# Performance work log

Hardware: AMD Instinct MI355X
Metric: run time of the kernel (lower is better)

Reference implementation:

```python
import jax, jax.numpy as jnp
import numpy as np

NUM_NODES = 100000
NUM_EDGES = 1600000
HID = 128
NODE_DIM = 5
MSG_DIM = 2


def _mlp(x, params):
    # 3 hidden ReLU layers + linear head, matching nn.Sequential in torch
    (W0, b0, W1, b1, W2, b2, W3, b3) = params
    h = jax.nn.relu(x @ W0 + b0)
    h = jax.nn.relu(h @ W1 + b1)
    h = jax.nn.relu(h @ W2 + b2)
    return h @ W3 + b3


def setup_inputs() -> dict:
    key = jax.random.key(0)
    ks = jax.random.split(key, 12)
    nodes = jax.random.normal(ks[0], (NUM_NODES, NODE_DIM), dtype=jnp.float32)
    edge_index = jax.random.randint(ks[1], (2, NUM_EDGES), 0, NUM_NODES, dtype=jnp.int32)

    def lin(k, fan_in, fan_out):
        # kaiming-uniform-ish init, scale irrelevant for correctness baseline
        bound = 1.0 / np.sqrt(fan_in)
        return jax.random.uniform(k, (fan_in, fan_out), jnp.float32, -bound, bound)

    return {
        "nodes": nodes,
        "edge_index": edge_index,
        "Wm0": lin(ks[2], 2 * NODE_DIM, HID), "bm0": jnp.zeros((HID,), jnp.float32),
        "Wm1": lin(ks[3], HID, HID),          "bm1": jnp.zeros((HID,), jnp.float32),
        "Wm2": lin(ks[4], HID, HID),          "bm2": jnp.zeros((HID,), jnp.float32),
        "Wm3": lin(ks[5], HID, MSG_DIM),      "bm3": jnp.zeros((MSG_DIM,), jnp.float32),
        "Wu0": lin(ks[6], NODE_DIM + MSG_DIM, HID), "bu0": jnp.zeros((HID,), jnp.float32),
        "Wu1": lin(ks[7], HID, HID),          "bu1": jnp.zeros((HID,), jnp.float32),
        "Wu2": lin(ks[8], HID, HID),          "bu2": jnp.zeros((HID,), jnp.float32),
        "Wu3": lin(ks[9], HID, MSG_DIM),      "bu3": jnp.zeros((MSG_DIM,), jnp.float32),
    }


def reference(nodes, edge_index, Wm0, bm0, Wm1, bm1, Wm2, bm2, Wm3, bm3,
              Wu0, bu0, Wu1, bu1, Wu2, bu2, Wu3, bu3):
    senders = edge_index[0]
    receivers = edge_index[1]
    # gather endpoints: [E, 2*node_dim]
    edge_inputs = jnp.concatenate([nodes[senders], nodes[receivers]], axis=-1)
    messages = _mlp(edge_inputs, (Wm0, bm0, Wm1, bm1, Wm2, bm2, Wm3, bm3))  # [E, msg_dim]
    # scatter-add pooling rho_{e->v}
    pooled = jax.ops.segment_sum(messages, receivers, num_segments=nodes.shape[0])  # [N, msg_dim]
    node_update_input = jnp.concatenate([nodes, pooled], axis=-1)  # [N, node_dim+msg_dim]
    delta_v = _mlp(node_update_input, (Wu0, bu0, Wu1, bu1, Wu2, bu2, Wu3, bu3))  # [N, 2]
    # Euler step on velocity columns 2:4
    updated = jnp.concatenate([nodes[:, :2], nodes[:, 2:4] + delta_v, nodes[:, 4:]], axis=-1)
    return updated
```

## Files before the change

kernel.cpp:

```cpp
#include <hip/hip_runtime.h>
#include <hip/hip_bf16.h>

#define NE 1600000
#define NN 100000
#define PSCALE 131072.0f

typedef __attribute__((ext_vector_type(8))) short s16x8;
typedef __attribute__((ext_vector_type(4))) float f32x4;
typedef __attribute__((ext_vector_type(16))) float f32x16;
typedef __attribute__((ext_vector_type(4))) int i32x4;
typedef __attribute__((ext_vector_type(4))) uint u32x4;

__device__ __forceinline__ ushort f2b(float v) {
  union { __hip_bfloat16 h; ushort u; } c; c.h = __float2bfloat16(v); return c.u;
}
__device__ __forceinline__ uint cvtpk(float a, float b) {
  uint r;
  asm("v_cvt_pk_bf16_f32 %0, %1, %2" : "=v"(r) : "v"(a), "v"(b));
  return r;
}
__device__ __forceinline__ uint pkrelu(float a, float b) {
  a = fmaxf(a, 0.f); b = fmaxf(b, 0.f);
  return cvtpk(a, b);
}
__device__ __forceinline__ f32x16 mfma32(s16x8 a, s16x8 b, f32x16 c) {
  return __builtin_amdgcn_mfma_f32_32x32x16_bf16(a, b, c, 0, 0, 0);
}
__device__ __forceinline__ u32x4 packg(const f32x16& a, int g) {
  u32x4 r;
#pragma unroll
  for (int w = 0; w < 4; w++) r[w] = pkrelu(a[8 * g + 2 * w], a[8 * g + 2 * w + 1]);
  return r;
}
__device__ __forceinline__ f32x16 loadbias(const float* bias, int mt, int hi) {
  f32x16 b;
#pragma unroll
  for (int q4 = 0; q4 < 4; q4++) {
    f32x4 v = *(const f32x4*)(bias + mt * 32 + q4 * 8 + hi * 4);
#pragma unroll
    for (int i = 0; i < 4; i++) b[q4 * 4 + i] = v[i];
  }
  return b;
}

__global__ void prep_weights(const float* s0, const float* s1, const float* s2, const float* s3,
                             const float* s4, const float* s5, const float* s6, const float* s7,
                             const float* bm0, const float* bu0, ushort* dst) {
  const int NFRAG[8] = {4, 32, 32, 8, 4, 32, 32, 8};
  const int offs[8]  = {0, 2048, 18432, 34816, 38912, 40960, 57344, 73728};
  const float* srcs[8] = {s0, s1, s2, s3, s4, s5, s6, s7};
  int b = blockIdx.x;
  int cnt = NFRAG[b] * 512;
  const float* src = srcs[b];
  bool isProducer = (b == 0 || b == 4);
  bool isHead = (b == 3 || b == 7);
  int F1 = (b < 4) ? 5 : 2;
  int kbias = (b < 4) ? 13 : 10;
  const float* bp = (b < 4) ? bm0 : bu0;
  ushort* d = dst + offs[b];
  for (int idx = threadIdx.x; idx < cnt; idx += blockDim.x) {
    int f = idx >> 9, r = idx & 511, lane = r >> 3, j = r & 7;
    int hi = lane >> 5, m = lane & 31;
    float v = 0.f;
    if (isProducer) {
      int ch = f * 32 + m;
      int k = hi * 8 + j;
      int row = -1;
      if (k < 5) row = k;
      else if (k >= 8 && k < 8 + F1) row = k - 3;
      if (row >= 0) v = src[row * 128 + ch];
      else if (k == kbias) v = bp[ch];
    } else {
      int s = isHead ? f : (f >> 2);
      int k = s * 16 + hi * 8 + j;
      int c = (k & ~12) | ((k & 4) << 1) | ((k & 8) >> 1);
      if (isHead) v = (m < 2) ? src[c * 2 + m] : 0.f;
      else {
        int ch = (f & 3) * 32 + m;
        v = src[c * 128 + ch];
      }
    }
    d[idx] = f2b(v);
  }
}

template <int MODE>
__global__ __launch_bounds__(512, 2)
void gnn_kernel(const float* __restrict__ nodes,
                const int* __restrict__ eidx,
                unsigned long long* __restrict__ pooled,
                const ushort* __restrict__ wsrc,
                const float* __restrict__ b1g, const float* __restrict__ b2g,
                const float* __restrict__ b3g,
                float* __restrict__ out) {
  __shared__ __align__(16) ushort wlds[36864];
  __shared__ __align__(16) float bias1[128];
  __shared__ __align__(16) float bias2[128];
  __shared__ __align__(16) float bias3[16];
  {
    i32x4* dw = (i32x4*)wlds;
    const i32x4* sw = (const i32x4*)wsrc;
    for (int i = threadIdx.x; i < 4608; i += 512) dw[i] = sw[256 + i];
    if (threadIdx.x < 128) {
      bias1[threadIdx.x] = b1g[threadIdx.x];
      bias2[threadIdx.x] = b2g[threadIdx.x];
    }
    if (threadIdx.x < 16) bias3[threadIdx.x] = (threadIdx.x < 2) ? b3g[threadIdx.x] : 0.f;
  }

  const int wv = threadIdx.x >> 6;
  const int l = threadIdx.x & 63;
  const int hi = l >> 5;
  const int e32 = l & 31;
  auto LF = [&](int base, int f) {
    return *(const s16x8*)(wlds + base + f * 512 + l * 8);
  };
  s16x8 w0p[4];
#pragma unroll
  for (int mt = 0; mt < 4; mt++)
    w0p[mt] = *(const s16x8*)(wsrc + ((mt * 64 + l) * 8));
  __syncthreads();

  int wid = blockIdx.x * 8 + wv;
  int nwv = gridDim.x * 8;
  const int NB = (MODE == 0) ? (NE / 32) : (NN / 32);
  const f32x16 z16 = {0.f, 0.f, 0.f, 0.f, 0.f, 0.f, 0.f, 0.f,
                      0.f, 0.f, 0.f, 0.f, 0.f, 0.f, 0.f, 0.f};

  float g0 = 0, g1 = 0, g2 = 0, g3 = 0, g4 = 0;
  auto PREF = [&](int bb) {
    if (bb < NB) {
      int e = (bb << 5) + e32;
      if (MODE == 0) {
        int idx = eidx[hi * NE + e];
        const float* np_ = nodes + idx * 5;
        g0 = np_[0]; g1 = np_[1]; g2 = np_[2]; g3 = np_[3]; g4 = np_[4];
      } else {
        if (hi == 0) {
          const float* np_ = nodes + e * 5;
          g0 = np_[0]; g1 = np_[1]; g2 = np_[2]; g3 = np_[3]; g4 = np_[4];
        } else {
          unsigned long long pl = pooled[e];
          int x32 = (int)(uint)pl;
          int y32 = (int)(pl >> 32) + (x32 < 0 ? 1 : 0);
          g0 = (float)x32 * (1.f / PSCALE);
          g1 = (float)y32 * (1.f / PSCALE);
        }
      }
    }
  };
  PREF(wid);

#pragma unroll 1
  for (int b = wid; b < NB; b += nwv) {
    const int rbase = b << 5;
    int rc = 0;
    if (MODE == 0) rc = eidx[NE + rbase + e32];
    s16x8 xf;
    {
      u32x4 f = {0u, 0u, 0u, 0u};
      if (MODE == 0) {
        f[0] = cvtpk(g0, g1); f[1] = cvtpk(g2, g3);
        f[2] = cvtpk(g4, hi ? 1.0f : 0.0f);
      } else {
        if (hi == 0) { f[0] = cvtpk(g0, g1); f[1] = cvtpk(g2, g3); f[2] = cvtpk(g4, 0.f); }
        else         { f[0] = cvtpk(g0, g1); f[1] = cvtpk(1.0f, 0.f); }
      }
      xf = __builtin_bit_cast(s16x8, f);
    }
    PREF(b + nwv);

    s16x8 wf[2][8];
#pragma unroll
    for (int s = 0; s < 8; s++) wf[0][s] = LF(0, s * 4);

    u32x4 phA[4][2];
    {
      f32x16 a;
      a = mfma32(w0p[0], xf, z16); phA[0][0] = packg(a, 0); phA[0][1] = packg(a, 1);
      a = mfma32(w0p[1], xf, z16); phA[1][0] = packg(a, 0); phA[1][1] = packg(a, 1);
      a = mfma32(w0p[2], xf, z16); phA[2][0] = packg(a, 0); phA[2][1] = packg(a, 1);
      a = mfma32(w0p[3], xf, z16); phA[3][0] = packg(a, 0); phA[3][1] = packg(a, 1);
    }
    u32x4 phB[4][2];
#pragma unroll
    for (int mt = 0; mt < 4; mt++) {
      if (mt < 3) {
#pragma unroll
        for (int s = 0; s < 8; s++) wf[(mt + 1) & 1][s] = LF(0, s * 4 + mt + 1);
      } else {
#pragma unroll
        for (int s = 0; s < 8; s++) wf[(mt + 1) & 1][s] = LF(16384, s * 4);
      }
      f32x16 a = loadbias(bias1, mt, hi);
#pragma unroll
      for (int s = 0; s < 8; s++)
        a = mfma32(wf[mt & 1][s], __builtin_bit_cast(s16x8, phA[s >> 1][s & 1]), a);
      phB[mt][0] = packg(a, 0);
      phB[mt][1] = packg(a, 1);
    }
    u32x4 phC[4][2];
#pragma unroll
    for (int mt = 0; mt < 4; mt++) {
      if (mt < 3) {
#pragma unroll
        for (int s = 0; s < 8; s++) wf[(mt + 1) & 1][s] = LF(16384, s * 4 + mt + 1);
      } else {
#pragma unroll
        for (int s = 0; s < 8; s++) wf[(mt + 1) & 1][s] = LF(32768, s);
      }
      f32x16 a = loadbias(bias2, mt, hi);
#pragma unroll
      for (int s = 0; s < 8; s++)
        a = mfma32(wf[mt & 1][s], __builtin_bit_cast(s16x8, phB[s >> 1][s & 1]), a);
      phC[mt][0] = packg(a, 0);
      phC[mt][1] = packg(a, 1);
    }
    f32x16 a = mfma32(wf[0][0], __builtin_bit_cast(s16x8, phC[0][0]), z16);
#pragma unroll
    for (int s = 1; s < 8; s++)
      a = mfma32(wf[0][s], __builtin_bit_cast(s16x8, phC[s >> 1][s & 1]), a);

    int e = rbase + e32;
    if (hi == 0) {
      float mv0 = a[0] + bias3[0], mv1 = a[1] + bias3[1];
      if (MODE == 0) {
        int ix = (int)rintf(mv0 * PSCALE);
        int iy = (int)rintf(mv1 * PSCALE);
        long long ad = (((long long)iy) << 32) + (long long)ix;
        atomicAdd(&pooled[rc], (unsigned long long)ad);
      } else {
        out[e * 5 + 2] = nodes[e * 5 + 2] + mv0;
        out[e * 5 + 3] = nodes[e * 5 + 3] + mv1;
      }
    } else if (MODE == 1) {
      out[e * 5 + 0] = nodes[e * 5 + 0];
      out[e * 5 + 1] = nodes[e * 5 + 1];
      out[e * 5 + 4] = nodes[e * 5 + 4];
    }
  }
}

extern "C" void kernel_launch(void* const* d_in, const int* in_sizes, int n_in,
                              void* d_out, int out_size, void* d_ws, size_t ws_size,
                              hipStream_t stream) {
  const float* nodes = (const float*)d_in[0];
  const int* eidx = (const int*)d_in[1];
  const float* Wm0 = (const float*)d_in[2];  const float* bm0 = (const float*)d_in[3];
  const float* Wm1 = (const float*)d_in[4];  const float* bm1 = (const float*)d_in[5];
  const float* Wm2 = (const float*)d_in[6];  const float* bm2 = (const float*)d_in[7];
  const float* Wm3 = (const float*)d_in[8];  const float* bm3 = (const float*)d_in[9];
  const float* Wu0 = (const float*)d_in[10]; const float* bu0 = (const float*)d_in[11];
  const float* Wu1 = (const float*)d_in[12]; const float* bu1 = (const float*)d_in[13];
  const float* Wu2 = (const float*)d_in[14]; const float* bu2 = (const float*)d_in[15];
  const float* Wu3 = (const float*)d_in[16]; const float* bu3 = (const float*)d_in[17];

  unsigned long long* pooled = (unsigned long long*)d_ws;
  ushort* wbuf = (ushort*)((char*)d_ws + 800000);

  hipMemsetAsync(pooled, 0, NN * 8, stream);
  prep_weights<<<8, 256, 0, stream>>>(Wm0, Wm1, Wm2, Wm3, Wu0, Wu1, Wu2, Wu3,
                                      bm0, bu0, wbuf);

  gnn_kernel<0><<<512, 512, 0, stream>>>(nodes, eidx, pooled, wbuf,
                                         bm1, bm2, bm3, nullptr);
  gnn_kernel<1><<<512, 512, 0, stream>>>(nodes, nullptr, pooled, wbuf + 38912,
                                         bu1, bu2, bu3, (float*)d_out);
}
```

Before: 166.9 us.

## Fuse pooled memset into weight prep, widen prep grid, skip LDS staging in node kernel

```diff
diff --git a/kernel.cpp b/kernel.cpp
--- a/kernel.cpp
+++ b/kernel.cpp
@@ -45,11 +45,18 @@
 
 __global__ void prep_weights(const float* s0, const float* s1, const float* s2, const float* s3,
                              const float* s4, const float* s5, const float* s6, const float* s7,
-                             const float* bm0, const float* bu0, ushort* dst) {
+                             const float* bm0, const float* bu0, ushort* dst,
+                             unsigned long long* pooled) {
+  if (blockIdx.x >= 64) {
+    for (int i = (blockIdx.x - 64) * 256 + threadIdx.x; i < NN; i += 16 * 256)
+      pooled[i] = 0ULL;
+    return;
+  }
   const int NFRAG[8] = {4, 32, 32, 8, 4, 32, 32, 8};
   const int offs[8]  = {0, 2048, 18432, 34816, 38912, 40960, 57344, 73728};
+  int part = blockIdx.x & 7;
+  int b = blockIdx.x >> 3;
   const float* srcs[8] = {s0, s1, s2, s3, s4, s5, s6, s7};
-  int b = blockIdx.x;
   int cnt = NFRAG[b] * 512;
   const float* src = srcs[b];
   bool isProducer = (b == 0 || b == 4);
@@ -58,7 +65,7 @@
   int kbias = (b < 4) ? 13 : 10;
   const float* bp = (b < 4) ? bm0 : bu0;
   ushort* d = dst + offs[b];
-  for (int idx = threadIdx.x; idx < cnt; idx += blockDim.x) {
+  for (int idx = part * 256 + threadIdx.x; idx < cnt; idx += 2048) {
     int f = idx >> 9, r = idx & 511, lane = r >> 3, j = r & 7;
     int hi = lane >> 5, m = lane & 31;
     float v = 0.f;
@@ -93,11 +100,11 @@
                 const float* __restrict__ b1g, const float* __restrict__ b2g,
                 const float* __restrict__ b3g,
                 float* __restrict__ out) {
-  __shared__ __align__(16) ushort wlds[36864];
-  __shared__ __align__(16) float bias1[128];
-  __shared__ __align__(16) float bias2[128];
-  __shared__ __align__(16) float bias3[16];
-  {
+  __shared__ __align__(16) ushort wlds[(MODE == 0) ? 36864 : 8];
+  __shared__ __align__(16) float bias1[(MODE == 0) ? 128 : 4];
+  __shared__ __align__(16) float bias2[(MODE == 0) ? 128 : 4];
+  __shared__ __align__(16) float bias3[(MODE == 0) ? 16 : 4];
+  if (MODE == 0) {
     i32x4* dw = (i32x4*)wlds;
     const i32x4* sw = (const i32x4*)wsrc;
     for (int i = threadIdx.x; i < 4608; i += 512) dw[i] = sw[256 + i];
@@ -112,14 +119,21 @@
   const int l = threadIdx.x & 63;
   const int hi = l >> 5;
   const int e32 = l & 31;
-  auto LF = [&](int base, int f) {
-    return *(const s16x8*)(wlds + base + f * 512 + l * 8);
+  auto LF = [&](int base, int f) -> s16x8 {
+    if (MODE == 0)
+      return *(const s16x8*)(wlds + base + f * 512 + l * 8);
+    else
+      return *(const s16x8*)(wsrc + 2048 + base + f * 512 + l * 8);
   };
   s16x8 w0p[4];
 #pragma unroll
   for (int mt = 0; mt < 4; mt++)
     w0p[mt] = *(const s16x8*)(wsrc + ((mt * 64 + l) * 8));
-  __syncthreads();
+  if (MODE == 0) __syncthreads();
+  const float* bb1 = (MODE == 0) ? (const float*)bias1 : b1g;
+  const float* bb2 = (MODE == 0) ? (const float*)bias2 : b2g;
+  const float b30 = (MODE == 0) ? bias3[0] : b3g[0];
+  const float b31 = (MODE == 0) ? bias3[1] : b3g[1];
 
   int wid = blockIdx.x * 8 + wv;
   int nwv = gridDim.x * 8;
@@ -192,7 +206,7 @@
 #pragma unroll
         for (int s = 0; s < 8; s++) wf[(mt + 1) & 1][s] = LF(16384, s * 4);
       }
-      f32x16 a = loadbias(bias1, mt, hi);
+      f32x16 a = loadbias(bb1, mt, hi);
 #pragma unroll
       for (int s = 0; s < 8; s++)
         a = mfma32(wf[mt & 1][s], __builtin_bit_cast(s16x8, phA[s >> 1][s & 1]), a);
@@ -209,7 +223,7 @@
 #pragma unroll
         for (int s = 0; s < 8; s++) wf[(mt + 1) & 1][s] = LF(32768, s);
       }
-      f32x16 a = loadbias(bias2, mt, hi);
+      f32x16 a = loadbias(bb2, mt, hi);
 #pragma unroll
       for (int s = 0; s < 8; s++)
         a = mfma32(wf[mt & 1][s], __builtin_bit_cast(s16x8, phB[s >> 1][s & 1]), a);
@@ -223,7 +237,7 @@
 
     int e = rbase + e32;
     if (hi == 0) {
-      float mv0 = a[0] + bias3[0], mv1 = a[1] + bias3[1];
+      float mv0 = a[0] + b30, mv1 = a[1] + b31;
       if (MODE == 0) {
         int ix = (int)rintf(mv0 * PSCALE);
         int iy = (int)rintf(mv1 * PSCALE);
@@ -258,12 +272,11 @@
   unsigned long long* pooled = (unsigned long long*)d_ws;
   ushort* wbuf = (ushort*)((char*)d_ws + 800000);
 
-  hipMemsetAsync(pooled, 0, NN * 8, stream);
-  prep_weights<<<8, 256, 0, stream>>>(Wm0, Wm1, Wm2, Wm3, Wu0, Wu1, Wu2, Wu3,
-                                      bm0, bu0, wbuf);
+  prep_weights<<<80, 256, 0, stream>>>(Wm0, Wm1, Wm2, Wm3, Wu0, Wu1, Wu2, Wu3,
+                                       bm0, bu0, wbuf, pooled);
 
   gnn_kernel<0><<<512, 512, 0, stream>>>(nodes, eidx, pooled, wbuf,
                                          bm1, bm2, bm3, nullptr);
-  gnn_kernel<1><<<512, 512, 0, stream>>>(nodes, nullptr, pooled, wbuf + 38912,
+  gnn_kernel<1><<<391, 512, 0, stream>>>(nodes, nullptr, pooled, wbuf + 38912,
                                          bu1, bu2, bu3, (float*)d_out);
 }
```

New measurement: 156.7 us (median of 3 runs). -6.1%, faster.
